# Kernel tuning notes

Measured on AMD Instinct MI355X. Metric: run time of the kernel, lower is better.

The kernel has to match this reference:

```python
import jax, jax.numpy as jnp
import numpy as np

D_MODEL = 256; D_FC = 1024; N_LEVELS = 4; N_HEADS = 8; N_POINTS = 4
D_HEAD = D_MODEL // N_HEADS
SPATIAL = np.array([[100, 100], [50, 50], [25, 25], [13, 13]], dtype=np.int64)
S_TOTAL = int((SPATIAL[:, 0] * SPATIAL[:, 1]).sum())  # 13294
BATCH = 2


def setup_inputs() -> dict:
    key = jax.random.key(0)
    ks = jax.random.split(key, 16)

    def lin(k, fi, fo):
        s = 1.0 / np.sqrt(fi)
        kw, kb = jax.random.split(k)
        W = jax.random.uniform(kw, (fi, fo), jnp.float32, -s, s)
        b = jax.random.uniform(kb, (fo,), jnp.float32, -s, s)
        return W, b

    W_off, b_off = lin(ks[0], D_MODEL, N_HEADS * N_LEVELS * N_POINTS * 2)
    W_attn, b_attn = lin(ks[1], D_MODEL, N_HEADS * N_LEVELS * N_POINTS)
    W_val, b_val = lin(ks[2], D_MODEL, D_MODEL)
    W_out, b_out = lin(ks[3], D_MODEL, D_MODEL)
    W1, b1 = lin(ks[4], D_MODEL, D_FC)
    W2, b2 = lin(ks[5], D_FC, D_MODEL)
    src = jax.random.normal(ks[6], (BATCH, S_TOTAL, D_MODEL), jnp.float32)
    pos = jax.random.normal(ks[7], (BATCH, S_TOTAL, D_MODEL), jnp.float32)
    reference_points = jax.random.uniform(ks[8], (BATCH, S_TOTAL, N_LEVELS, 2), jnp.float32)
    level_start_index = np.concatenate([[0], np.cumsum(SPATIAL[:, 0] * SPATIAL[:, 1])[:-1]]).astype(np.int64)
    return dict(src=src, pos=pos, reference_points=reference_points,
                spatial_shapes=SPATIAL, level_start_index=level_start_index,
                W_off=W_off, b_off=b_off, W_attn=W_attn, b_attn=b_attn,
                W_val=W_val, b_val=b_val, W_out=W_out, b_out=b_out,
                ln1_g=jnp.ones(D_MODEL, jnp.float32), ln1_b=jnp.zeros(D_MODEL, jnp.float32),
                W1=W1, b1=b1, W2=W2, b2=b2,
                ln2_g=jnp.ones(D_MODEL, jnp.float32), ln2_b=jnp.zeros(D_MODEL, jnp.float32))


def layernorm(x, g, b, eps=1e-5):
    mu = x.mean(-1, keepdims=True)
    var = ((x - mu) ** 2).mean(-1, keepdims=True)
    return (x - mu) * jax.lax.rsqrt(var + eps) * g + b


def ms_deform_attn(query, value_in, ref_pts, shapes,
                   W_off, b_off, W_attn, b_attn, W_val, b_val, W_out, b_out):
    N, Lq, _ = query.shape
    value = (value_in @ W_val + b_val).reshape(N, -1, N_HEADS, D_HEAD)
    off = (query @ W_off + b_off).reshape(N, Lq, N_HEADS, N_LEVELS, N_POINTS, 2)
    attn = (query @ W_attn + b_attn).reshape(N, Lq, N_HEADS, N_LEVELS * N_POINTS)
    attn = jax.nn.softmax(attn, -1).reshape(N, Lq, N_HEADS, N_LEVELS, N_POINTS)
    # offset normalizer is (W_l, H_l) per level
    norm = jnp.array([[w, h] for (h, w) in shapes], dtype=query.dtype)
    loc = ref_pts[:, :, None, :, None, :] + off / norm[None, None, None, :, None, :]
    out = jnp.zeros((N, Lq, N_HEADS, D_HEAD), query.dtype)
    start = 0
    for l, (H_, W_) in enumerate(shapes):
        v = value[:, start:start + H_ * W_].transpose(0, 2, 1, 3)  # [N, heads, HW, d]
        start += H_ * W_
        loc_l = loc[:, :, :, l]  # [N, Lq, heads, P, 2]
        # grid_sample(align_corners=False, padding_mode='zeros'): pixel = loc*size - 0.5
        px = loc_l[..., 0] * W_ - 0.5
        py = loc_l[..., 1] * H_ - 0.5
        x0 = jnp.floor(px); y0 = jnp.floor(py)
        wx = (px - x0)[..., None]; wy = (py - y0)[..., None]
        x0i = x0.astype(jnp.int32); y0i = y0.astype(jnp.int32)

        def samp(xi, yi):
            valid = (xi >= 0) & (xi < W_) & (yi >= 0) & (yi < H_)
            idx = jnp.clip(yi, 0, H_ - 1) * W_ + jnp.clip(xi, 0, W_ - 1)  # [N,Lq,heads,P]
            idx = idx.transpose(0, 2, 1, 3).reshape(N, N_HEADS, Lq * N_POINTS, 1)
            g = jnp.take_along_axis(v, idx, axis=2)  # [N,heads,Lq*P,d]
            g = g.reshape(N, N_HEADS, Lq, N_POINTS, D_HEAD).transpose(0, 2, 1, 3, 4)
            return g * valid[..., None]

        val = (samp(x0i, y0i) * (1 - wx) * (1 - wy)
               + samp(x0i + 1, y0i) * wx * (1 - wy)
               + samp(x0i, y0i + 1) * (1 - wx) * wy
               + samp(x0i + 1, y0i + 1) * wx * wy)  # [N,Lq,heads,P,d]
        out = out + (val * attn[:, :, :, l, :, None]).sum(3)
    return out.reshape(N, Lq, D_MODEL) @ W_out + b_out


def reference(src, pos, reference_points, spatial_shapes, level_start_index,
              W_off, b_off, W_attn, b_attn, W_val, b_val, W_out, b_out,
              ln1_g, ln1_b, W1, b1, W2, b2, ln2_g, ln2_b):
    shapes = [(int(spatial_shapes[l, 0]), int(spatial_shapes[l, 1])) for l in range(N_LEVELS)]
    q = src + pos
    attn_out = ms_deform_attn(q, src, reference_points, shapes,
                              W_off, b_off, W_attn, b_attn, W_val, b_val, W_out, b_out)
    x = layernorm(src + attn_out, ln1_g, ln1_b)  # dropout is identity in eval
    ffn = jax.nn.relu(x @ W1 + b1) @ W2 + b2
    return layernorm(x + ffn, ln2_g, ln2_b)
```

## Files before the change

### kernel.cpp

```cpp
#include <hip/hip_runtime.h>
#include <hip/hip_bf16.h>

#define DM 256
#define STOT 13294
#define MTOT (2 * STOT)

using bf16 = __hip_bfloat16;
typedef __attribute__((ext_vector_type(8))) short short8;
typedef __attribute__((ext_vector_type(4))) float floatx4;

#define GLDS16(g, l) __builtin_amdgcn_global_load_lds( \
    (const __attribute__((address_space(1))) void*)(g), \
    (__attribute__((address_space(3))) void*)(l), 16, 0, 0)

__device__ __forceinline__ float bu2f(unsigned u) { return __uint_as_float(u << 16); }
__device__ __forceinline__ unsigned short f2bu(float f) {
    union { bf16 h; unsigned short u; } c; c.h = __float2bfloat16(f); return c.u;
}

__global__ void detect_dtype(const unsigned* g1, int* flag) {
    if (threadIdx.x == 0 && blockIdx.x == 0)
        *flag = (g1[0] == 0x3F800000u) ? 1 : 0;
}

struct PW { const void* W[6]; const void* B[10]; };

__global__ void prep_weights(PW a, bf16* __restrict__ WT, float* __restrict__ bf,
                             const int* __restrict__ flag) {
    const long id = (long)blockIdx.x * 256 + threadIdx.x;
    const bool f32in = (*flag != 0);
    const int sz[6]  = {65536, 65536, 32768, 65536, 262144, 262144};
    const int Ns[6]  = {256, 256, 128, 256, 1024, 256};
    const int Ksh[6] = {8, 8, 8, 8, 8, 10};
    if (id < 753664) {
        long e = id; int j = 0;
        while (e >= sz[j]) { e -= sz[j]; ++j; }
        const int n = (int)(e >> Ksh[j]);
        const int k = (int)(e & ((1 << Ksh[j]) - 1));
        const size_t src = (size_t)k * Ns[j] + n;
        float v = f32in ? ((const float*)a.W[j])[src] : __bfloat162float(((const bf16*)a.W[j])[src]);
        WT[id] = __float2bfloat16(v);
    } else if (id < 753664 + 3200) {
        long e = id - 753664; int j = 0;
        const int bsz[10] = {256, 256, 128, 256, 1024, 256, 256, 256, 256, 256};
        while (e >= bsz[j]) { e -= bsz[j]; ++j; }
        float v = f32in ? ((const float*)a.B[j])[e] : __bfloat162float(((const bf16*)a.B[j])[e]);
        bf[id - 753664] = v;
    }
}

__global__ void prep_act(const void* __restrict__ src, const void* __restrict__ pos,
                         bf16* __restrict__ sbf, bf16* __restrict__ qbf,
                         const int* __restrict__ flag) {
    const long i = ((long)blockIdx.x * 256 + threadIdx.x) * 8;
    if (i >= (long)MTOT * DM) return;
    unsigned short ps[8], pq[8];
    if (*flag) {
        const float* s = (const float*)src + i;
        const float* p = (const float*)pos + i;
        float4 a0 = *(const float4*)s, a1 = *(const float4*)(s + 4);
        float4 b0 = *(const float4*)p, b1 = *(const float4*)(p + 4);
        const float av[8] = {a0.x, a0.y, a0.z, a0.w, a1.x, a1.y, a1.z, a1.w};
        const float bv[8] = {b0.x, b0.y, b0.z, b0.w, b1.x, b1.y, b1.z, b1.w};
#pragma unroll
        for (int j = 0; j < 8; ++j) { ps[j] = f2bu(av[j]); pq[j] = f2bu(av[j] + bv[j]); }
    } else {
        const unsigned short* s = (const unsigned short*)src + i;
        const unsigned short* p = (const unsigned short*)pos + i;
        uint4 a = *(const uint4*)s, b = *(const uint4*)p;
        const unsigned* ua = (const unsigned*)&a;
        const unsigned* ub = (const unsigned*)&b;
#pragma unroll
        for (int j = 0; j < 4; ++j) {
            float a0 = bu2f(ua[j] & 0xffffu), a1 = bu2f(ua[j] >> 16);
            float b0 = bu2f(ub[j] & 0xffffu), b1 = bu2f(ub[j] >> 16);
            ps[j * 2] = f2bu(a0); ps[j * 2 + 1] = f2bu(a1);
            pq[j * 2] = f2bu(a0 + b0); pq[j * 2 + 1] = f2bu(a1 + b1);
        }
    }
    *(uint4*)((unsigned short*)sbf + i) = *(const uint4*)ps;
    *(uint4*)((unsigned short*)qbf + i) = *(const uint4*)pq;
}

template<bool RELU>
__global__ __launch_bounds__(256, 4)
void gemm_bf16(const bf16* __restrict__ A0, const bf16* __restrict__ A1, int n_a0,
               const bf16* __restrict__ WT, const float* __restrict__ bias,
               bf16* __restrict__ C0, bf16* __restrict__ C1, bf16* __restrict__ C2,
               int M, int N, int K, int ldc0) {
    __shared__ __align__(16) bf16 sh[16384];
    const int t = threadIdx.x;
    const int wave = t >> 6, lane = t & 63;
    const int bm = blockIdx.y * 128, bn = blockIdx.x * 128;
    const bf16* __restrict__ A = (bn < n_a0) ? A0 : A1;
    const int wm = (wave >> 1) * 64, wn = (wave & 1) * 64;
    const int l15 = lane & 15, quad = lane >> 4;
    const int srow = lane >> 2, sko = (lane & 3) * 8;

    floatx4 acc[4][4];
#pragma unroll
    for (int i = 0; i < 4; ++i)
#pragma unroll
        for (int j = 0; j < 4; ++j) acc[i][j] = (floatx4)0.f;

    const int nb = K >> 5;
#pragma unroll
    for (int rh = 0; rh < 2; ++rh) {
        const int rbase = rh * 64 + wave * 16;
        const int gm = min(bm + rbase + srow, M - 1);
        GLDS16(A + (size_t)gm * K + sko, &sh[rbase * 32]);
        GLDS16(WT + (size_t)(bn + rbase + srow) * K + sko, &sh[8192 + rbase * 32]);
    }
    for (int i = 0; i < nb; ++i) {
        __syncthreads();
        if (i + 1 < nb) {
            const int k0 = (i + 1) << 5;
            const int bo = ((i + 1) & 1) * 4096;
#pragma unroll
            for (int rh = 0; rh < 2; ++rh) {
                const int rbase = rh * 64 + wave * 16;
                const int gm = min(bm + rbase + srow, M - 1);
                GLDS16(A + (size_t)gm * K + k0 + sko, &sh[bo + rbase * 32]);
                GLDS16(WT + (size_t)(bn + rbase + srow) * K + k0 + sko, &sh[8192 + bo + rbase * 32]);
            }
        }
        const int bo = (i & 1) * 4096;
        short8 af[4], bfr[4];
#pragma unroll
        for (int mi = 0; mi < 4; ++mi)
            af[mi] = *(const short8*)&sh[bo + (wm + mi * 16 + l15) * 32 + quad * 8];
#pragma unroll
        for (int nj = 0; nj < 4; ++nj)
            bfr[nj] = *(const short8*)&sh[8192 + bo + (wn + nj * 16 + l15) * 32 + quad * 8];
#pragma unroll
        for (int mi = 0; mi < 4; ++mi)
#pragma unroll
            for (int nj = 0; nj < 4; ++nj)
                acc[mi][nj] = __builtin_amdgcn_mfma_f32_16x16x32_bf16(bfr[nj], af[mi], acc[mi][nj], 0, 0, 0);
    }

    bf16* C = C0; int coloff = bn, ldc = ldc0;
    if (C1 != nullptr && bn >= 256) {
        if (C2 != nullptr && bn >= 512) { C = C2; coloff = bn - 512; ldc = 128; }
        else                            { C = C1; coloff = bn - 256; ldc = 256; }
    }
    float4 bv4[4];
#pragma unroll
    for (int nj = 0; nj < 4; ++nj)
        bv4[nj] = *(const float4*)&bias[bn + wn + nj * 16 + quad * 4];
#pragma unroll
    for (int mi = 0; mi < 4; ++mi) {
        const int gm = bm + wm + mi * 16 + l15;
        if (gm >= M) continue;
#pragma unroll
        for (int nj = 0; nj < 4; ++nj) {
            const float bb[4] = {bv4[nj].x, bv4[nj].y, bv4[nj].z, bv4[nj].w};
            unsigned short pk[4];
#pragma unroll
            for (int r = 0; r < 4; ++r) {
                float v = acc[mi][nj][r] + bb[r];
                if (RELU) v = fmaxf(v, 0.f);
                pk[r] = f2bu(v);
            }
            *(uint2*)&C[(size_t)gm * ldc + coloff + wn + nj * 16 + quad * 4] = *(const uint2*)pk;
        }
    }
}

__global__ void softmax16(bf16* __restrict__ a, int total) {
    const int i = blockIdx.x * 256 + threadIdx.x;
    if (i >= total) return;
    unsigned short* p = (unsigned short*)(a + (size_t)i * 16);
    uint4 r0 = *(const uint4*)p, r1 = *(const uint4*)(p + 8);
    float w[16];
    const unsigned* u0 = (const unsigned*)&r0;
    const unsigned* u1 = (const unsigned*)&r1;
#pragma unroll
    for (int j = 0; j < 4; ++j) {
        w[j * 2] = bu2f(u0[j] & 0xffffu); w[j * 2 + 1] = bu2f(u0[j] >> 16);
        w[8 + j * 2] = bu2f(u1[j] & 0xffffu); w[8 + j * 2 + 1] = bu2f(u1[j] >> 16);
    }
    float mx = -1e30f;
#pragma unroll
    for (int j = 0; j < 16; ++j) mx = fmaxf(mx, w[j]);
    float s = 0.f;
#pragma unroll
    for (int j = 0; j < 16; ++j) { w[j] = __expf(w[j] - mx); s += w[j]; }
    const float inv = 1.f / s;
    unsigned short pk[16];
#pragma unroll
    for (int j = 0; j < 16; ++j) pk[j] = f2bu(w[j] * inv);
    *(uint4*)p = *(const uint4*)pk;
    *(uint4*)(p + 8) = *(const uint4*)(pk + 8);
}

__global__ __launch_bounds__(256)
void deform_sample(const bf16* __restrict__ value, const bf16* __restrict__ off,
                   const bf16* __restrict__ attw, const void* __restrict__ refp,
                   bf16* __restrict__ out, const int* __restrict__ flag) {
    __shared__ int4   sIdx[512];
    __shared__ float4 sWt[512];
    const int t = threadIdx.x;
    const bool f32r = (*flag != 0);

#pragma unroll
    for (int r = 0; r < 2; ++r) {
        const int e = t + r * 256;
        const int ql = e >> 7, rem = e & 127;
        const int h = rem & 7, j = rem >> 3;
        const int l = j >> 2;
        const int q = blockIdx.x * 4 + ql;
        const int b = (q >= STOT) ? 1 : 0;
        const int Ws4[4] = {100, 50, 25, 13};
        const int Ls4[4] = {0, 10000, 12500, 13125};

        const unsigned op = *(const unsigned*)((const unsigned short*)off + (size_t)q * 256 + h * 32 + j * 2);
        const float ox = bu2f(op & 0xffffu), oy = bu2f(op >> 16);
        const float aw = bu2f(((const unsigned short*)attw)[(size_t)q * 128 + h * 16 + j]);
        float rx, ry;
        if (f32r) {
            const float* rp = (const float*)refp + (size_t)q * 8 + l * 2;
            rx = rp[0]; ry = rp[1];
        } else {
            const unsigned short* rp = (const unsigned short*)refp + (size_t)q * 8 + l * 2;
            rx = bu2f(rp[0]); ry = bu2f(rp[1]);
        }
        const int W_ = Ws4[l];
        const float fw = (float)W_;
        const float px = rx * fw + ox - 0.5f;
        const float py = ry * fw + oy - 0.5f;
        const float x0f = floorf(px), y0f = floorf(py);
        const float wx = px - x0f, wy = py - y0f;
        const int x0 = (int)x0f, y0 = (int)y0f;
        const float ex = 1.f - wx, ey = 1.f - wy;
        const int rowb = b * STOT + Ls4[l];
        const int xs[2] = {x0, x0 + 1}, ys[2] = {y0, y0 + 1};
        const float fx[2] = {ex, wx}, fy[2] = {ey, wy};
        int idxv[4]; float wv[4];
#pragma unroll
        for (int cy = 0; cy < 2; ++cy)
#pragma unroll
            for (int cx = 0; cx < 2; ++cx) {
                const int xi = xs[cx], yi = ys[cy];
                const bool valid = (xi >= 0) & (xi < W_) & (yi >= 0) & (yi < W_);
                const int xc = min(max(xi, 0), W_ - 1);
                const int yc = min(max(yi, 0), W_ - 1);
                idxv[cy * 2 + cx] = (rowb + yc * W_ + xc) << 9;
                wv[cy * 2 + cx] = valid ? fx[cx] * fy[cy] * aw : 0.f;
            }
        const int slot = ql * 128 + rem;
        sIdx[slot] = make_int4(idxv[0], idxv[1], idxv[2], idxv[3]);
        sWt[slot] = make_float4(wv[0], wv[1], wv[2], wv[3]);
    }
    __syncthreads();

    const int ql = t >> 6, ln = t & 63;
    const int h = ln >> 3, dg = ln & 7;
    const int q = blockIdx.x * 4 + ql;
    const char* vbytes = (const char*)value;
    const unsigned laneoff = (unsigned)((h * 32 + dg * 4) * 2);
    const int sbase = ql * 128 + h;
    float a0 = 0.f, a1 = 0.f, a2 = 0.f, a3 = 0.f;
#pragma unroll 4
    for (int j = 0; j < 16; ++j) {
        const int4 iv = sIdx[sbase + j * 8];
        const float4 wv = sWt[sbase + j * 8];
        const int iarr[4] = {iv.x, iv.y, iv.z, iv.w};
        const float warr[4] = {wv.x, wv.y, wv.z, wv.w};
#pragma unroll
        for (int c = 0; c < 4; ++c) {
            const unsigned bo = (unsigned)iarr[c] + laneoff;
            const uint2 v = *(const uint2*)(vbytes + bo);
            a0 = fmaf(warr[c], __uint_as_float(v.x << 16), a0);
            a1 = fmaf(warr[c], __uint_as_float(v.x & 0xffff0000u), a1);
            a2 = fmaf(warr[c], __uint_as_float(v.y << 16), a2);
            a3 = fmaf(warr[c], __uint_as_float(v.y & 0xffff0000u), a3);
        }
    }
    unsigned short pk[4] = {f2bu(a0), f2bu(a1), f2bu(a2), f2bu(a3)};
    *(ushort4*)((unsigned short*)out + (size_t)q * 256 + h * 32 + dg * 4) = *(const ushort4*)pk;
}

__global__ __launch_bounds__(512, 1)
void out_ln1(const bf16* __restrict__ vsamp, const bf16* __restrict__ srcbf,
             const bf16* __restrict__ WoT, const float* __restrict__ bo_f,
             const float* __restrict__ g1, const float* __restrict__ be1,
             bf16* __restrict__ vx, int M) {
    __shared__ __align__(16) bf16 Bs[8 * 4096];
    const int t = threadIdx.x, wave = t >> 6, lane = t & 63;
    const int l15 = lane & 15, quad = lane >> 4;
    const int srow = lane >> 2, sko = (lane & 3) * 8;
    const int bm = blockIdx.x * 128;
    const int mrow = bm + wave * 16 + l15;
    const int mc = min(mrow, M - 1);

    short8 af[8];
#pragma unroll
    for (int kk = 0; kk < 8; ++kk)
        af[kk] = *(const short8*)(vsamp + (size_t)mc * 256 + kk * 32 + quad * 8);

    floatx4 acc[16];
#pragma unroll
    for (int i = 0; i < 16; ++i) acc[i] = (floatx4)0.f;

    for (int nc = 0; nc < 2; ++nc) {
        __syncthreads();
#pragma unroll
        for (int rr = 0; rr < 8; ++rr)
            GLDS16(WoT + (size_t)(nc * 128 + rr * 16 + srow) * 256 + wave * 32 + sko,
                   &Bs[wave * 4096 + rr * 512]);
        __syncthreads();
#pragma unroll
        for (int kk = 0; kk < 8; ++kk)
#pragma unroll
            for (int nj = 0; nj < 8; ++nj) {
                short8 bfr = *(const short8*)&Bs[kk * 4096 + (nj * 16 + l15) * 32 + quad * 8];
                acc[nc * 8 + nj] = __builtin_amdgcn_mfma_f32_16x16x32_bf16(bfr, af[kk], acc[nc * 8 + nj], 0, 0, 0);
            }
    }

    float s = 0.f;
#pragma unroll
    for (int nj = 0; nj < 16; ++nj) {
        const int n = nj * 16 + quad * 4;
        const float4 bo = *(const float4*)&bo_f[n];
        const uint2 ru = *(const uint2*)(srcbf + (size_t)mc * 256 + n);
        const float rs[4] = {bu2f(ru.x & 0xffffu), bu2f(ru.x >> 16), bu2f(ru.y & 0xffffu), bu2f(ru.y >> 16)};
        const float bb[4] = {bo.x, bo.y, bo.z, bo.w};
#pragma unroll
        for (int r = 0; r < 4; ++r) { acc[nj][r] += bb[r] + rs[r]; s += acc[nj][r]; }
    }
    s += __shfl_xor(s, 16, 64); s += __shfl_xor(s, 32, 64);
    const float mean = s * (1.f / 256.f);
    float s2 = 0.f;
#pragma unroll
    for (int nj = 0; nj < 16; ++nj)
#pragma unroll
        for (int r = 0; r < 4; ++r) { const float c = acc[nj][r] - mean; s2 += c * c; }
    s2 += __shfl_xor(s2, 16, 64); s2 += __shfl_xor(s2, 32, 64);
    const float rstd = rsqrtf(s2 * (1.f / 256.f) + 1e-5f);
    if (mrow < M) {
#pragma unroll
        for (int nj = 0; nj < 16; ++nj) {
            const int n = nj * 16 + quad * 4;
            const float4 g = *(const float4*)&g1[n];
            const float4 b = *(const float4*)&be1[n];
            const float gg[4] = {g.x, g.y, g.z, g.w}, bb[4] = {b.x, b.y, b.z, b.w};
            unsigned short pk[4];
#pragma unroll
            for (int r = 0; r < 4; ++r) pk[r] = f2bu((acc[nj][r] - mean) * rstd * gg[r] + bb[r]);
            *(uint2*)&vx[(size_t)mrow * 256 + n] = *(const uint2*)pk;
        }
    }
}

__global__ __launch_bounds__(256, 2)
void ffn_ln2(const bf16* __restrict__ vx, const bf16* __restrict__ W1T, const bf16* __restrict__ W2T,
             const float* __restrict__ b1f, const float* __restrict__ b2f,
             const float* __restrict__ g2, const float* __restrict__ be2,
             void* __restrict__ outp, const int* __restrict__ flag, int M) {
    __shared__ __align__(16) bf16 Bs1[16384];
    __shared__ __align__(16) bf16 Bs2[8192];
    __shared__ __align__(16) bf16 Hs[64 * 136];
    __shared__ float2 red[128];
    const int t = threadIdx.x, wv = t >> 6, lane = t & 63;
    const int l15 = lane & 15, quad = lane >> 4;
    const int g = wv & 1, nh = wv >> 1;
    const int srow = lane >> 2, sko = (lane & 3) * 8;
    const int bm = blockIdx.x * 64;

    int mrow[2], mc[2];
#pragma unroll
    for (int mi = 0; mi < 2; ++mi) {
        mrow[mi] = bm + g * 32 + mi * 16 + l15;
        mc[mi] = min(mrow[mi], M - 1);
    }
    short8 af[2][8];
#pragma unroll
    for (int mi = 0; mi < 2; ++mi)
#pragma unroll
        for (int kk = 0; kk < 8; ++kk)
            af[mi][kk] = *(const short8*)(vx + (size_t)mc[mi] * 256 + kk * 32 + quad * 8);

    floatx4 acc2[2][8];
#pragma unroll
    for (int mi = 0; mi < 2; ++mi)
#pragma unroll
        for (int nj = 0; nj < 8; ++nj) acc2[mi][nj] = (floatx4)0.f;

    for (int ch = 0; ch < 8; ++ch) {
        floatx4 acc1[2][4];
#pragma unroll
        for (int mi = 0; mi < 2; ++mi)
#pragma unroll
            for (int nj = 0; nj < 4; ++nj) acc1[mi][nj] = (floatx4)0.f;
#pragma unroll
        for (int ks = 0; ks < 2; ++ks) {
            __syncthreads();
#pragma unroll
            for (int j = 0; j < 8; ++j)
                GLDS16(W1T + (size_t)(ch * 128 + j * 16 + srow) * 256 + ks * 128 + wv * 32 + sko,
                       &Bs1[wv * 4096 + j * 512]);
            __syncthreads();
#pragma unroll
            for (int kk = 0; kk < 4; ++kk) {
                short8 bfr[4];
#pragma unroll
                for (int nj = 0; nj < 4; ++nj)
                    bfr[nj] = *(const short8*)&Bs1[kk * 4096 + (nh * 64 + nj * 16 + l15) * 32 + quad * 8];
#pragma unroll
                for (int mi = 0; mi < 2; ++mi)
#pragma unroll
                    for (int nj = 0; nj < 4; ++nj)
                        acc1[mi][nj] = __builtin_amdgcn_mfma_f32_16x16x32_bf16(bfr[nj], af[mi][ks * 4 + kk], acc1[mi][nj], 0, 0, 0);
            }
        }
#pragma unroll
        for (int mi = 0; mi < 2; ++mi)
#pragma unroll
            for (int nj = 0; nj < 4; ++nj) {
                const int kl = nh * 64 + nj * 16 + quad * 4;
                const float4 bb = *(const float4*)&b1f[ch * 128 + kl];
                const float bv[4] = {bb.x, bb.y, bb.z, bb.w};
                unsigned short pk[4];
#pragma unroll
                for (int r = 0; r < 4; ++r) pk[r] = f2bu(fmaxf(acc1[mi][nj][r] + bv[r], 0.f));
                *(uint2*)&Hs[(g * 32 + mi * 16 + l15) * 136 + kl] = *(const uint2*)pk;
            }
#pragma unroll
        for (int p = 0; p < 4; ++p) {
            __syncthreads();
#pragma unroll
            for (int j = 0; j < 4; ++j)
                GLDS16(W2T + (size_t)(wv * 64 + j * 16 + srow) * 1024 + ch * 128 + p * 32 + sko,
                       &Bs2[(wv * 64 + j * 16) * 32]);
            __syncthreads();
            short8 ah[2];
#pragma unroll
            for (int mi = 0; mi < 2; ++mi)
                ah[mi] = *(const short8*)&Hs[(g * 32 + mi * 16 + l15) * 136 + p * 32 + quad * 8];
#pragma unroll
            for (int nj = 0; nj < 8; ++nj) {
                short8 bfr = *(const short8*)&Bs2[(nh * 128 + nj * 16 + l15) * 32 + quad * 8];
#pragma unroll
                for (int mi = 0; mi < 2; ++mi)
                    acc2[mi][nj] = __builtin_amdgcn_mfma_f32_16x16x32_bf16(bfr, ah[mi], acc2[mi][nj], 0, 0, 0);
            }
        }
    }

    float sm[2] = {0.f, 0.f}, sq[2] = {0.f, 0.f};
#pragma unroll
    for (int mi = 0; mi < 2; ++mi)
#pragma unroll
        for (int nj = 0; nj < 8; ++nj) {
            const int n = nh * 128 + nj * 16 + quad * 4;
            const float4 bo = *(const float4*)&b2f[n];
            const uint2 ru = *(const uint2*)(vx + (size_t)mc[mi] * 256 + n);
            const float rs[4] = {bu2f(ru.x & 0xffffu), bu2f(ru.x >> 16), bu2f(ru.y & 0xffffu), bu2f(ru.y >> 16)};
            const float bb[4] = {bo.x, bo.y, bo.z, bo.w};
#pragma unroll
            for (int r = 0; r < 4; ++r) {
                const float v = acc2[mi][nj][r] + bb[r] + rs[r];
                acc2[mi][nj][r] = v; sm[mi] += v; sq[mi] += v * v;
            }
        }
#pragma unroll
    for (int mi = 0; mi < 2; ++mi) {
        sm[mi] += __shfl_xor(sm[mi], 16, 64); sm[mi] += __shfl_xor(sm[mi], 32, 64);
        sq[mi] += __shfl_xor(sq[mi], 16, 64); sq[mi] += __shfl_xor(sq[mi], 32, 64);
    }
    __syncthreads();
    if (quad == 0) {
#pragma unroll
        for (int mi = 0; mi < 2; ++mi)
            red[((nh * 2 + g) * 2 + mi) * 16 + l15] = make_float2(sm[mi], sq[mi]);
    }
    __syncthreads();
    const bool f32o = (*flag != 0);
#pragma unroll
    for (int mi = 0; mi < 2; ++mi) {
        const float2 o = red[(((1 - nh) * 2 + g) * 2 + mi) * 16 + l15];
        const float ts = sm[mi] + o.x, tq = sq[mi] + o.y;
        const float mean = ts * (1.f / 256.f);
        const float var = tq * (1.f / 256.f) - mean * mean;
        const float rstd = rsqrtf(var + 1e-5f);
        if (mrow[mi] < M) {
#pragma unroll
            for (int nj = 0; nj < 8; ++nj) {
                const int n = nh * 128 + nj * 16 + quad * 4;
                const float4 gv = *(const float4*)&g2[n];
                const float4 bv = *(const float4*)&be2[n];
                const float gg[4] = {gv.x, gv.y, gv.z, gv.w}, bb[4] = {bv.x, bv.y, bv.z, bv.w};
                float y[4];
#pragma unroll
                for (int r = 0; r < 4; ++r) y[r] = (acc2[mi][nj][r] - mean) * rstd * gg[r] + bb[r];
                if (f32o) {
                    float4 ov = {y[0], y[1], y[2], y[3]};
                    *(float4*)((float*)outp + (size_t)mrow[mi] * 256 + n) = ov;
                } else {
                    unsigned short pk[4] = {f2bu(y[0]), f2bu(y[1]), f2bu(y[2]), f2bu(y[3])};
                    *(uint2*)((bf16*)outp + (size_t)mrow[mi] * 256 + n) = *(const uint2*)pk;
                }
            }
        }
    }
}

extern "C" void kernel_launch(void* const* d_in, const int* in_sizes, int n_in,
                              void* d_out, int out_size, void* d_ws, size_t ws_size,
                              hipStream_t stream) {
    const void* src   = d_in[0];
    const void* pos   = d_in[1];
    const void* refp  = d_in[2];
    const void* W_off = d_in[5];
    const void* b_off = d_in[6];
    const void* W_att = d_in[7];
    const void* b_att = d_in[8];
    const void* W_val = d_in[9];
    const void* b_val = d_in[10];
    const void* W_out = d_in[11];
    const void* b_out = d_in[12];
    const void* ln1g  = d_in[13];
    const void* ln1b  = d_in[14];
    const void* W1    = d_in[15];
    const void* b1    = d_in[16];
    const void* W2    = d_in[17];
    const void* b2    = d_in[18];
    const void* ln2g  = d_in[19];
    const void* ln2b  = d_in[20];

    const size_t M = MTOT;
    bf16* src_bf = (bf16*)d_ws;
    bf16* q_bf   = src_bf + M * 256;
    bf16* v_val  = src_bf + M * 512;
    bf16* v_off  = src_bf + M * 768;
    bf16* v_attn = src_bf + M * 1024;
    bf16* v_samp = src_bf + M * 1152;
    bf16* v_x    = src_bf + M * 1408;
    bf16* WT     = src_bf + M * 1664;
    float* biasf = (float*)(WT + 753664);
    int* flag    = (int*)(biasf + 3200);

    dim3 blk(256);
    const int mg = (MTOT + 127) / 128;

    detect_dtype<<<1, 64, 0, stream>>>((const unsigned*)ln1g, flag);

    PW pw;
    pw.W[0] = W_val; pw.W[1] = W_off; pw.W[2] = W_att; pw.W[3] = W_out; pw.W[4] = W1; pw.W[5] = W2;
    pw.B[0] = b_val; pw.B[1] = b_off; pw.B[2] = b_att; pw.B[3] = b_out; pw.B[4] = b1; pw.B[5] = b2;
    pw.B[6] = ln1g;  pw.B[7] = ln1b;  pw.B[8] = ln2g;  pw.B[9] = ln2b;
    prep_weights<<<(753664 + 3200 + 255) / 256, blk, 0, stream>>>(pw, WT, biasf, flag);
    prep_act<<<(int)((M * 256 / 8 + 255) / 256), blk, 0, stream>>>(src, pos, src_bf, q_bf, flag);

    gemm_bf16<false><<<dim3(5, mg), blk, 0, stream>>>(src_bf, q_bf, 256, WT, biasf,
                                                      v_val, v_off, v_attn, MTOT, 640, 256, 256);
    softmax16<<<(MTOT * 8 + 255) / 256, blk, 0, stream>>>(v_attn, MTOT * 8);
    deform_sample<<<MTOT / 4, blk, 0, stream>>>(v_val, v_off, v_attn, refp, v_samp, flag);
    out_ln1<<<mg, dim3(512), 0, stream>>>(v_samp, src_bf, WT + 163840, biasf + 640,
                                          biasf + 2176, biasf + 2432, v_x, MTOT);
    ffn_ln2<<<(MTOT + 63) / 64, blk, 0, stream>>>(v_x, WT + 229376, WT + 491520,
                                                  biasf + 896, biasf + 1920,
                                                  biasf + 2688, biasf + 2944,
                                                  d_out, flag, MTOT);
}
```

Before: 326.6 us.

## Store value projection head-major and gather 16-byte rows in deformable sampling

The value GEMM epilogue now writes its output in a head-major layout, [head][row][32 channels], so each sampled corner for one head is a contiguous 64-byte row. The sampling kernel splits each head's corners between two lane halves, loads 16 bytes per lane instead of 8, and combines the partial sums with a cross-lane shuffle. The aim is fewer, wider and more cache-friendly gather loads per sampling point. In exchange, the GEMM epilogue does strided transposed stores and the sampler does extra shuffle work.

```diff
diff --git a/kernel.cpp b/kernel.cpp
--- a/kernel.cpp
+++ b/kernel.cpp
@@ -87,7 +87,7 @@
 void gemm_bf16(const bf16* __restrict__ A0, const bf16* __restrict__ A1, int n_a0,
                const bf16* __restrict__ WT, const float* __restrict__ bias,
                bf16* __restrict__ C0, bf16* __restrict__ C1, bf16* __restrict__ C2,
-               int M, int N, int K, int ldc0) {
+               int M, int N, int K, int ldc0, int vtM) {
     __shared__ __align__(16) bf16 sh[16384];
     const int t = threadIdx.x;
     const int wave = t >> 6, lane = t & 63;
@@ -139,10 +139,12 @@
                 acc[mi][nj] = __builtin_amdgcn_mfma_f32_16x16x32_bf16(bfr[nj], af[mi], acc[mi][nj], 0, 0, 0);
     }
 
-    bf16* C = C0; int coloff = bn, ldc = ldc0;
+    bf16* C = C0; int coloff = bn, ldc = ldc0; bool vt = false;
     if (C1 != nullptr && bn >= 256) {
         if (C2 != nullptr && bn >= 512) { C = C2; coloff = bn - 512; ldc = 128; }
         else                            { C = C1; coloff = bn - 256; ldc = 256; }
+    } else {
+        vt = (vtM > 0);
     }
     float4 bv4[4];
 #pragma unroll
@@ -162,7 +164,12 @@
                 if (RELU) v = fmaxf(v, 0.f);
                 pk[r] = f2bu(v);
             }
-            *(uint2*)&C[(size_t)gm * ldc + coloff + wn + nj * 16 + quad * 4] = *(const uint2*)pk;
+            const int n = coloff + wn + nj * 16 + quad * 4;
+            if (vt) {
+                *(uint2*)&C[((size_t)(n >> 5) * vtM + gm) * 32 + (n & 31)] = *(const uint2*)pk;
+            } else {
+                *(uint2*)&C[(size_t)gm * ldc + n] = *(const uint2*)pk;
+            }
         }
     }
 }
@@ -195,7 +202,7 @@
 }
 
 __global__ __launch_bounds__(256)
-void deform_sample(const bf16* __restrict__ value, const bf16* __restrict__ off,
+void deform_sample(const bf16* __restrict__ valueT, const bf16* __restrict__ off,
                    const bf16* __restrict__ attw, const void* __restrict__ refp,
                    bf16* __restrict__ out, const int* __restrict__ flag) {
     __shared__ int4   sIdx[512];
@@ -233,7 +240,7 @@
         const float wx = px - x0f, wy = py - y0f;
         const int x0 = (int)x0f, y0 = (int)y0f;
         const float ex = 1.f - wx, ey = 1.f - wy;
-        const int rowb = b * STOT + Ls4[l];
+        const int rowb = h * MTOT + b * STOT + Ls4[l];
         const int xs[2] = {x0, x0 + 1}, ys[2] = {y0, y0 + 1};
         const float fx[2] = {ex, wx}, fy[2] = {ey, wy};
         int idxv[4]; float wv[4];
@@ -245,7 +252,7 @@
                 const bool valid = (xi >= 0) & (xi < W_) & (yi >= 0) & (yi < W_);
                 const int xc = min(max(xi, 0), W_ - 1);
                 const int yc = min(max(yi, 0), W_ - 1);
-                idxv[cy * 2 + cx] = (rowb + yc * W_ + xc) << 9;
+                idxv[cy * 2 + cx] = (rowb + yc * W_ + xc) << 6;
                 wv[cy * 2 + cx] = valid ? fx[cx] * fy[cy] * aw : 0.f;
             }
         const int slot = ql * 128 + rem;
@@ -256,29 +263,48 @@
 
     const int ql = t >> 6, ln = t & 63;
     const int h = ln >> 3, dg = ln & 7;
+    const int side = dg >> 2, cg = dg & 3;
     const int q = blockIdx.x * 4 + ql;
-    const char* vbytes = (const char*)value;
-    const unsigned laneoff = (unsigned)((h * 32 + dg * 4) * 2);
+    const char* vbytes = (const char*)valueT;
+    const unsigned lo = (unsigned)(cg * 16);
     const int sbase = ql * 128 + h;
-    float a0 = 0.f, a1 = 0.f, a2 = 0.f, a3 = 0.f;
-#pragma unroll 4
-    for (int j = 0; j < 16; ++j) {
-        const int4 iv = sIdx[sbase + j * 8];
-        const float4 wv = sWt[sbase + j * 8];
-        const int iarr[4] = {iv.x, iv.y, iv.z, iv.w};
-        const float warr[4] = {wv.x, wv.y, wv.z, wv.w};
-#pragma unroll
-        for (int c = 0; c < 4; ++c) {
-            const unsigned bo = (unsigned)iarr[c] + laneoff;
-            const uint2 v = *(const uint2*)(vbytes + bo);
-            a0 = fmaf(warr[c], __uint_as_float(v.x << 16), a0);
-            a1 = fmaf(warr[c], __uint_as_float(v.x & 0xffff0000u), a1);
-            a2 = fmaf(warr[c], __uint_as_float(v.y << 16), a2);
-            a3 = fmaf(warr[c], __uint_as_float(v.y & 0xffff0000u), a3);
-        }
-    }
-    unsigned short pk[4] = {f2bu(a0), f2bu(a1), f2bu(a2), f2bu(a3)};
-    *(ushort4*)((unsigned short*)out + (size_t)q * 256 + h * 32 + dg * 4) = *(const ushort4*)pk;
+
+    float acc[8];
+#pragma unroll
+    for (int i = 0; i < 8; ++i) acc[i] = 0.f;
+
+#pragma unroll 2
+    for (int jc = 0; jc < 4; ++jc) {
+        uint4 vd[8]; float wgt[8];
+#pragma unroll
+        for (int u = 0; u < 4; ++u) {
+            const int j = jc * 4 + u;
+            const int4 iv = sIdx[sbase + j * 8];
+            const float4 wv = sWt[sbase + j * 8];
+            const int ia = side ? iv.y : iv.x;
+            const int ib = side ? iv.w : iv.z;
+            vd[u * 2]     = *(const uint4*)(vbytes + (unsigned)ia + lo);
+            vd[u * 2 + 1] = *(const uint4*)(vbytes + (unsigned)ib + lo);
+            wgt[u * 2]     = side ? wv.y : wv.x;
+            wgt[u * 2 + 1] = side ? wv.w : wv.z;
+        }
+#pragma unroll
+        for (int u = 0; u < 8; ++u) {
+            const unsigned* pv = (const unsigned*)&vd[u];
+            const float wq = wgt[u];
+#pragma unroll
+            for (int c = 0; c < 4; ++c) {
+                acc[c * 2]     = fmaf(wq, __uint_as_float(pv[c] << 16), acc[c * 2]);
+                acc[c * 2 + 1] = fmaf(wq, __uint_as_float(pv[c] & 0xffff0000u), acc[c * 2 + 1]);
+            }
+        }
+    }
+#pragma unroll
+    for (int i = 0; i < 8; ++i) acc[i] += __shfl_xor(acc[i], 4, 64);
+    unsigned short pk[4];
+#pragma unroll
+    for (int r = 0; r < 4; ++r) pk[r] = f2bu(acc[side * 4 + r]);
+    *(uint2*)((unsigned short*)out + (size_t)q * 256 + h * 32 + cg * 8 + side * 4) = *(const uint2*)pk;
 }
 
 __global__ __launch_bounds__(512, 1)
@@ -555,7 +581,7 @@
     prep_act<<<(int)((M * 256 / 8 + 255) / 256), blk, 0, stream>>>(src, pos, src_bf, q_bf, flag);
 
     gemm_bf16<false><<<dim3(5, mg), blk, 0, stream>>>(src_bf, q_bf, 256, WT, biasf,
-                                                      v_val, v_off, v_attn, MTOT, 640, 256, 256);
+                                                      v_val, v_off, v_attn, MTOT, 640, 256, 256, MTOT);
     softmax16<<<(MTOT * 8 + 255) / 256, blk, 0, stream>>>(v_attn, MTOT * 8);
     deform_sample<<<MTOT / 4, blk, 0, stream>>>(v_val, v_off, v_attn, refp, v_samp, flag);
     out_ln1<<<mg, dim3(512), 0, stream>>>(v_samp, src_bf, WT + 163840, biasf + 640,
```

After: 313.6 us. -4.0%, faster.
